# Kernel optimization log

Hardware: AMD Instinct MI355X
Metric: run time of the kernel (lower is better)

Reference implementation:

```python
import jax, jax.numpy as jnp
import numpy as np

EMBED_DIM = 1024
NUM_HEADS = 16
HEAD_DIM = EMBED_DIM // NUM_HEADS


def setup_inputs() -> dict:
    key = jax.random.key(0)
    k_x, k_wqkv, k_bqkv, k_wo, k_bo = jax.random.split(key, 5)
    B, T, C = 8, 1024, EMBED_DIM
    s = 1.0 / np.sqrt(C)
    return {
        "x": jax.random.normal(k_x, (B, T, C), dtype=jnp.float32),
        "W_qkv": jax.random.uniform(k_wqkv, (C, 3 * C), minval=-s, maxval=s, dtype=jnp.float32),
        "b_qkv": jax.random.uniform(k_bqkv, (3 * C,), minval=-s, maxval=s, dtype=jnp.float32),
        "W_out": jax.random.uniform(k_wo, (C, C), minval=-s, maxval=s, dtype=jnp.float32),
        "b_out": jax.random.uniform(k_bo, (C,), minval=-s, maxval=s, dtype=jnp.float32),
    }


def reference(x, W_qkv, b_qkv, W_out, b_out):
    B, T, C = x.shape
    H, D = NUM_HEADS, HEAD_DIM
    qkv = x @ W_qkv + b_qkv                      # [B,T,3C]
    q, k, v = jnp.split(qkv, 3, axis=-1)
    q = q.reshape(B, T, H, D).transpose(0, 2, 1, 3)  # [B,H,T,D]
    k = k.reshape(B, T, H, D).transpose(0, 2, 1, 3)
    v = v.reshape(B, T, H, D).transpose(0, 2, 1, 3)
    scores = jnp.einsum("bhqd,bhkd->bhqk", q, k) / np.sqrt(D).astype(np.float32)
    causal = jnp.tril(jnp.ones((T, T), dtype=bool))
    scores = jnp.where(causal[None, None], scores, -jnp.inf)
    attn = jax.nn.softmax(scores, axis=-1)       # dropout is identity in eval
    out = jnp.einsum("bhqk,bhkd->bhqd", attn, v)
    out = out.transpose(0, 2, 1, 3).reshape(B, T, C)
    return out @ W_out + b_out
```

## Files before the change

kernel.cpp:

```cpp
#include <hip/hip_runtime.h>
#include <hip/hip_bf16.h>
#include <cstdint>

using bf16 = __hip_bfloat16;
typedef short short8 __attribute__((ext_vector_type(8)));
typedef float floatx4 __attribute__((ext_vector_type(4)));

__device__ __forceinline__ void async_load16(const bf16* g, bf16* l) {
    __builtin_amdgcn_global_load_lds(
        (const __attribute__((address_space(1))) uint32_t*)g,
        (__attribute__((address_space(3))) uint32_t*)l, 16, 0, 0);
}

__device__ __forceinline__ uint32_t pack2(float a, float b) {
    union { bf16 h[2]; uint32_t u; } p;
    p.h[0] = __float2bfloat16(a);
    p.h[1] = __float2bfloat16(b);
    return p.u;
}

__global__ __launch_bounds__(256)
void cvt_bf16_kernel(const float* __restrict__ in, bf16* __restrict__ out) {
    const int i = (blockIdx.x * 256 + threadIdx.x) * 4;
    const float4 v = *(const float4*)(in + i);
    bf16 o[4] = {__float2bfloat16(v.x), __float2bfloat16(v.y),
                 __float2bfloat16(v.z), __float2bfloat16(v.w)};
    *(ushort4*)(out + i) = *(ushort4*)o;
}

__global__ __launch_bounds__(256)
void transpose_cvt_kernel(const float* __restrict__ in, bf16* __restrict__ out,
                          int R, int C) {
    __shared__ float tile[32][33];
    const int tx = threadIdx.x & 31, ty = threadIdx.x >> 5;
    const int c0 = blockIdx.x * 32, r0 = blockIdx.y * 32;
    #pragma unroll
    for (int i = 0; i < 32; i += 8)
        tile[ty + i][tx] = in[(size_t)(r0 + ty + i) * C + c0 + tx];
    __syncthreads();
    #pragma unroll
    for (int i = 0; i < 32; i += 8)
        out[(size_t)(c0 + ty + i) * R + r0 + tx] = __float2bfloat16(tile[tx][ty + i]);
}

template <int MODE>
__global__ __launch_bounds__(256, 2)
void gemm_bt_kernel(const bf16* __restrict__ A, const bf16* __restrict__ Bt,
                    const float* __restrict__ bias, int K,
                    bf16* __restrict__ q_ws, bf16* __restrict__ k_ws,
                    bf16* __restrict__ vt_ws, float* __restrict__ out, int N) {
    __shared__ bf16 As[128 * 32];
    __shared__ bf16 Bs[128 * 32];
    const int tid = threadIdx.x;
    const int wave = tid >> 6, lane = tid & 63;
    const int ln = lane & 15, quad = lane >> 4;
    const int wm = wave & 1, wn = wave >> 1;
    const int m0 = blockIdx.y * 128, n0 = blockIdx.x * 128;

    floatx4 acc[4][4] = {};

    for (int k0 = 0; k0 < K; k0 += 32) {
        __syncthreads();
        #pragma unroll
        for (int c = 0; c < 2; ++c) {
            const int e = (c * 256 + tid) * 8;
            async_load16(A + (size_t)(m0 + (e >> 5)) * K + k0 + (e & 31),
                         &As[(c * 256 + wave * 64) * 8]);
        }
        #pragma unroll
        for (int c = 0; c < 2; ++c) {
            const int e = (c * 256 + tid) * 8;
            async_load16(Bt + (size_t)(n0 + (e >> 5)) * K + k0 + (e & 31),
                         &Bs[(c * 256 + wave * 64) * 8]);
        }
        __syncthreads();

        short8 af[4], bfr[4];
        #pragma unroll
        for (int i = 0; i < 4; ++i) {
            af[i]  = *(const short8*)&As[(wm * 64 + i * 16 + ln) * 32 + quad * 8];
            bfr[i] = *(const short8*)&Bs[(wn * 64 + i * 16 + ln) * 32 + quad * 8];
        }
        #pragma unroll
        for (int mi = 0; mi < 4; ++mi)
            #pragma unroll
            for (int ni = 0; ni < 4; ++ni)
                acc[mi][ni] = __builtin_amdgcn_mfma_f32_16x16x32_bf16(
                    af[mi], bfr[ni], acc[mi][ni], 0, 0, 0);
    }

    #pragma unroll
    for (int ni = 0; ni < 4; ++ni) {
        const int col = n0 + wn * 64 + ni * 16 + ln;
        const float bv = bias[col];
        if (MODE == 0) {
            const int which = col >> 10;
            const int cc = col & 1023;
            const int h = cc >> 6, d = cc & 63;
            #pragma unroll
            for (int mi = 0; mi < 4; ++mi) {
                const int rowb = m0 + wm * 64 + mi * 16 + quad * 4;
                if (which == 2) {
                    const int bb = rowb >> 10, t = rowb & 1023;
                    const int tl = t & 63;
                    const int tt = (t & ~63) + ((((tl >> 3) ^ (d & 7)) << 3) | (tl & 7));
                    uint2 w2 = { pack2(acc[mi][ni][0] + bv, acc[mi][ni][1] + bv),
                                 pack2(acc[mi][ni][2] + bv, acc[mi][ni][3] + bv) };
                    *(uint2*)&vt_ws[((size_t)(bb * 16 + h) * 64 + d) * 1024 + tt] = w2;
                } else {
                    bf16* dst = (which == 0) ? q_ws : k_ws;
                    #pragma unroll
                    for (int r = 0; r < 4; ++r) {
                        const int row = rowb + r;
                        const int bb = row >> 10, t = row & 1023;
                        float v = acc[mi][ni][r] + bv;
                        if (which == 0) v *= 0.1803368801111601f;
                        const int dd = (((d >> 3) ^ (t & 7)) << 3) | (d & 7);
                        dst[((size_t)(bb * 16 + h) * 1024 + t) * 64 + dd] =
                            __float2bfloat16(v);
                    }
                }
            }
        } else {
            #pragma unroll
            for (int mi = 0; mi < 4; ++mi) {
                const int rowb = m0 + wm * 64 + mi * 16 + quad * 4;
                #pragma unroll
                for (int r = 0; r < 4; ++r)
                    out[(size_t)(rowb + r) * N + col] = acc[mi][ni][r] + bv;
            }
        }
    }
}

__global__ __launch_bounds__(256, 3)
void attn_kernel(const bf16* __restrict__ Q, const bf16* __restrict__ K,
                 const bf16* __restrict__ Vt, bf16* __restrict__ O) {
    constexpr int T = 1024;
    __shared__ bf16 QPs[128 * 64];
    __shared__ bf16 Ks[2][64 * 64];
    __shared__ bf16 Vts[2][64 * 64];

    const int bh = blockIdx.y;
    const int tid = threadIdx.x;
    const int wave = tid >> 6, lane = tid & 63;
    const int ln = lane & 15, quad = lane >> 4;

    const bf16* Kg = K + (size_t)bh * T * 64;
    const bf16* Vg = Vt + (size_t)bh * 64 * T;
    const int b = bh >> 4, h = bh & 15;

    #pragma unroll
    for (int phase = 0; phase < 2; ++phase) {
        const int jt = phase ? 7 - blockIdx.x : blockIdx.x;
        const int q0 = jt * 128;
        const int nkt = 2 * jt + 2;

        const bf16* Qg = Q + (size_t)bh * T * 64 + (size_t)q0 * 64;
        #pragma unroll
        for (int c = 0; c < 4; ++c)
            async_load16(Qg + (size_t)(c * 256 + tid) * 8,
                         &QPs[(c * 256 + wave * 64) * 8]);
        #pragma unroll
        for (int c = 0; c < 2; ++c)
            async_load16(Kg + (size_t)(c * 256 + tid) * 8,
                         &Ks[0][(c * 256 + wave * 64) * 8]);
        #pragma unroll
        for (int c = 0; c < 2; ++c) {
            const int e = (c * 256 + tid) * 8;
            async_load16(Vg + (size_t)(e >> 6) * T + (e & 63),
                         &Vts[0][(c * 256 + wave * 64) * 8]);
        }
        __syncthreads();

        short8 bq[2][2];
        #pragma unroll
        for (int qj = 0; qj < 2; ++qj)
            #pragma unroll
            for (int ks = 0; ks < 2; ++ks) {
                const int row = wave * 32 + qj * 16 + ln;
                const int ch = (ks * 4 + quad) ^ (row & 7);
                bq[qj][ks] = *(const short8*)&QPs[row * 64 + ch * 8];
            }

        floatx4 oacc[4][2] = {};
        float rm[2] = {-1e30f, -1e30f}, rl[2] = {0.f, 0.f};
        const int qbw = q0 + wave * 32;

        for (int kt = 0; kt < nkt; ++kt) {
            const int cur = kt & 1;
            if (kt + 1 < nkt) {
                const int nxt = cur ^ 1;
                #pragma unroll
                for (int c = 0; c < 2; ++c)
                    async_load16(Kg + (size_t)(kt + 1) * 4096 + (size_t)(c * 256 + tid) * 8,
                                 &Ks[nxt][(c * 256 + wave * 64) * 8]);
                #pragma unroll
                for (int c = 0; c < 2; ++c) {
                    const int e = (c * 256 + tid) * 8;
                    async_load16(Vg + (size_t)(e >> 6) * T + (kt + 1) * 64 + (e & 63),
                                 &Vts[nxt][(c * 256 + wave * 64) * 8]);
                }
            }

            const int k0 = kt * 64;
            if (k0 <= qbw + 31) {
                const bool tail = (k0 + 63 > qbw);

                floatx4 sacc[4][2] = {};
                #pragma unroll
                for (int nj = 0; nj < 4; ++nj) {
                    if (tail && k0 + nj * 16 > qbw + 31) continue;
                    short8 ak[2];
                    #pragma unroll
                    for (int ks = 0; ks < 2; ++ks) {
                        const int row = nj * 16 + ln;
                        const int ch = (ks * 4 + quad) ^ (row & 7);
                        ak[ks] = *(const short8*)&Ks[cur][row * 64 + ch * 8];
                    }
                    #pragma unroll
                    for (int qj = 0; qj < 2; ++qj) {
                        if (tail && k0 + nj * 16 > qbw + qj * 16 + 15) continue;
                        #pragma unroll
                        for (int ks = 0; ks < 2; ++ks)
                            sacc[nj][qj] = __builtin_amdgcn_mfma_f32_16x16x32_bf16(
                                ak[ks], bq[qj][ks], sacc[nj][qj], 0, 0, 0);
                    }
                }

                if (tail) {
                    #pragma unroll
                    for (int nj = 0; nj < 4; ++nj)
                        #pragma unroll
                        for (int qj = 0; qj < 2; ++qj) {
                            const int qq = qbw + qj * 16 + ln;
                            #pragma unroll
                            for (int r = 0; r < 4; ++r) {
                                const int kk = k0 + nj * 16 + quad * 4 + r;
                                if (kk > qq) sacc[nj][qj][r] = -1e30f;
                            }
                        }
                }

                #pragma unroll
                for (int qj = 0; qj < 2; ++qj) {
                    float mx = sacc[0][qj][0];
                    #pragma unroll
                    for (int nj = 0; nj < 4; ++nj)
                        #pragma unroll
                        for (int r = 0; r < 4; ++r) mx = fmaxf(mx, sacc[nj][qj][r]);
                    mx = fmaxf(mx, __shfl_xor(mx, 16, 64));
                    mx = fmaxf(mx, __shfl_xor(mx, 32, 64));
                    const float mn = fmaxf(rm[qj], mx);
                    const float alpha = exp2f(rm[qj] - mn);
                    rm[qj] = mn;
                    rl[qj] *= alpha;
                    #pragma unroll
                    for (int dt = 0; dt < 4; ++dt) oacc[dt][qj] *= alpha;
                    float rs = 0.f;
                    const int qrow = wave * 32 + qj * 16 + ln;
                    #pragma unroll
                    for (int nj = 0; nj < 4; ++nj) {
                        float p[4];
                        #pragma unroll
                        for (int r = 0; r < 4; ++r) {
                            p[r] = exp2f(sacc[nj][qj][r] - mn);
                            rs += p[r];
                        }
                        const int kcol = nj * 16 + quad * 4;
                        const int ch = (kcol >> 3) ^ (qrow & 7);
                        uint2 w2 = { pack2(p[0], p[1]), pack2(p[2], p[3]) };
                        *(uint2*)&QPs[qrow * 64 + ch * 8 + (kcol & 7)] = w2;
                    }
                    rl[qj] += rs;
                }

                #pragma unroll
                for (int ks4 = 0; ks4 < 2; ++ks4) {
                    short8 bp[2];
                    #pragma unroll
                    for (int qj = 0; qj < 2; ++qj) {
                        const int qrow = wave * 32 + qj * 16 + ln;
                        const int ch = (ks4 * 4 + quad) ^ (qrow & 7);
                        bp[qj] = *(const short8*)&QPs[qrow * 64 + ch * 8];
                    }
                    #pragma unroll
                    for (int dt = 0; dt < 4; ++dt) {
                        const int row = dt * 16 + ln;
                        const int ch = (ks4 * 4 + quad) ^ (row & 7);
                        const short8 av = *(const short8*)&Vts[cur][row * 64 + ch * 8];
                        #pragma unroll
                        for (int qj = 0; qj < 2; ++qj)
                            oacc[dt][qj] = __builtin_amdgcn_mfma_f32_16x16x32_bf16(
                                av, bp[qj], oacc[dt][qj], 0, 0, 0);
                    }
                }
            }

            __syncthreads();
        }

        #pragma unroll
        for (int qj = 0; qj < 2; ++qj) {
            float l = rl[qj];
            l += __shfl_xor(l, 16, 64);
            l += __shfl_xor(l, 32, 64);
            const float inv = 1.0f / l;
            const int t = q0 + wave * 32 + qj * 16 + ln;
            const size_t rowb = ((size_t)b * 1024 + t) * 1024 + h * 64;
            #pragma unroll
            for (int dt = 0; dt < 4; ++dt) {
                uint2 w2 = { pack2(oacc[dt][qj][0] * inv, oacc[dt][qj][1] * inv),
                             pack2(oacc[dt][qj][2] * inv, oacc[dt][qj][3] * inv) };
                *(uint2*)&O[rowb + dt * 16 + quad * 4] = w2;
            }
        }
    }
}

extern "C" void kernel_launch(void* const* d_in, const int* in_sizes, int n_in,
                              void* d_out, int out_size, void* d_ws, size_t ws_size,
                              hipStream_t stream) {
    const float* x     = (const float*)d_in[0];
    const float* W_qkv = (const float*)d_in[1];
    const float* b_qkv = (const float*)d_in[2];
    const float* W_out = (const float*)d_in[3];
    const float* b_out = (const float*)d_in[4];
    float* out = (float*)d_out;

    char* ws = (char*)d_ws;
    const size_t MB = 1u << 20;
    bf16* x_bf   = (bf16*)(ws + 0);
    bf16* wqkv_t = (bf16*)(ws + 16 * MB);
    bf16* wout_t = (bf16*)(ws + 22 * MB);
    bf16* q_ws   = (bf16*)(ws + 24 * MB);
    bf16* k_ws   = (bf16*)(ws + 40 * MB);
    bf16* vt_ws  = (bf16*)(ws + 56 * MB);
    bf16* ao_ws  = (bf16*)(ws + 72 * MB);

    cvt_bf16_kernel<<<8192, 256, 0, stream>>>(x, x_bf);
    transpose_cvt_kernel<<<dim3(96, 32), 256, 0, stream>>>(W_qkv, wqkv_t, 1024, 3072);
    transpose_cvt_kernel<<<dim3(32, 32), 256, 0, stream>>>(W_out, wout_t, 1024, 1024);

    gemm_bt_kernel<0><<<dim3(24, 64), 256, 0, stream>>>(
        x_bf, wqkv_t, b_qkv, 1024, q_ws, k_ws, vt_ws, nullptr, 3072);

    attn_kernel<<<dim3(4, 128), 256, 0, stream>>>(q_ws, k_ws, vt_ws, ao_ws);

    gemm_bt_kernel<1><<<dim3(8, 64), 256, 0, stream>>>(
        ao_ws, wout_t, b_out, 1024, nullptr, nullptr, nullptr, out, 1024);
}
```

Before: 252.2 us.

## Double-buffer GEMM tiles, split QKV GEMM, transpose operands for vectorized epilogues

Adds double-buffered LDS staging to the GEMM, using explicit vmcnt/lgkmcnt waits and barriers so the next K tile loads while the current one computes. It also uses the same waits in place of __syncthreads in the attention loop. The QKV projection is split into a Q/K GEMM with swapped operands, computing the transposed product so each lane writes four consecutive head-dim elements as one packed store, plus a separate V GEMM. The output projection is swapped the same way to emit float4 stores. The cost is an extra kernel launch, doubled LDS for the GEMM, and fragile hand-placed wait counts that must match the number of outstanding async loads.

```diff
diff --git a/kernel.cpp b/kernel.cpp
--- a/kernel.cpp
+++ b/kernel.cpp
@@ -5,11 +5,23 @@
 using bf16 = __hip_bfloat16;
 typedef short short8 __attribute__((ext_vector_type(8)));
 typedef float floatx4 __attribute__((ext_vector_type(4)));
+
+#define QSCALE 0.1803368801111601f
 
 __device__ __forceinline__ void async_load16(const bf16* g, bf16* l) {
     __builtin_amdgcn_global_load_lds(
         (const __attribute__((address_space(1))) uint32_t*)g,
         (__attribute__((address_space(3))) uint32_t*)l, 16, 0, 0);
+}
+
+__device__ __forceinline__ void bar_lgkm0() {
+    asm volatile("s_waitcnt lgkmcnt(0)\ns_barrier" ::: "memory");
+}
+__device__ __forceinline__ void bar_vm4() {
+    asm volatile("s_waitcnt vmcnt(4)\ns_barrier" ::: "memory");
+}
+__device__ __forceinline__ void bar_vm0() {
+    asm volatile("s_waitcnt vmcnt(0)\ns_barrier" ::: "memory");
 }
 
 __device__ __forceinline__ uint32_t pack2(float a, float b) {
@@ -44,13 +56,13 @@
 }
 
 template <int MODE>
-__global__ __launch_bounds__(256, 2)
+__global__ __launch_bounds__(256, 4)
 void gemm_bt_kernel(const bf16* __restrict__ A, const bf16* __restrict__ Bt,
                     const float* __restrict__ bias, int K,
-                    bf16* __restrict__ q_ws, bf16* __restrict__ k_ws,
-                    bf16* __restrict__ vt_ws, float* __restrict__ out, int N) {
-    __shared__ bf16 As[128 * 32];
-    __shared__ bf16 Bs[128 * 32];
+                    bf16* __restrict__ o0, bf16* __restrict__ o1,
+                    float* __restrict__ fout) {
+    __shared__ bf16 As[2][128 * 32];
+    __shared__ bf16 Bs[2][128 * 32];
     const int tid = threadIdx.x;
     const int wave = tid >> 6, lane = tid & 63;
     const int ln = lane & 15, quad = lane >> 4;
@@ -58,28 +70,48 @@
     const int m0 = blockIdx.y * 128, n0 = blockIdx.x * 128;
 
     floatx4 acc[4][4] = {};
-
-    for (int k0 = 0; k0 < K; k0 += 32) {
-        __syncthreads();
-        #pragma unroll
-        for (int c = 0; c < 2; ++c) {
-            const int e = (c * 256 + tid) * 8;
-            async_load16(A + (size_t)(m0 + (e >> 5)) * K + k0 + (e & 31),
-                         &As[(c * 256 + wave * 64) * 8]);
-        }
-        #pragma unroll
-        for (int c = 0; c < 2; ++c) {
-            const int e = (c * 256 + tid) * 8;
-            async_load16(Bt + (size_t)(n0 + (e >> 5)) * K + k0 + (e & 31),
-                         &Bs[(c * 256 + wave * 64) * 8]);
-        }
-        __syncthreads();
+    const int nkt = K >> 5;
+
+    #pragma unroll
+    for (int c = 0; c < 2; ++c) {
+        const int e = (c * 256 + tid) * 8;
+        async_load16(A + (size_t)(m0 + (e >> 5)) * K + (e & 31),
+                     &As[0][(c * 256 + wave * 64) * 8]);
+    }
+    #pragma unroll
+    for (int c = 0; c < 2; ++c) {
+        const int e = (c * 256 + tid) * 8;
+        async_load16(Bt + (size_t)(n0 + (e >> 5)) * K + (e & 31),
+                     &Bs[0][(c * 256 + wave * 64) * 8]);
+    }
+
+    for (int kt = 0; kt < nkt; ++kt) {
+        const int cur = kt & 1;
+        bar_lgkm0();
+        if (kt + 1 < nkt) {
+            const int k0 = (kt + 1) << 5;
+            #pragma unroll
+            for (int c = 0; c < 2; ++c) {
+                const int e = (c * 256 + tid) * 8;
+                async_load16(A + (size_t)(m0 + (e >> 5)) * K + k0 + (e & 31),
+                             &As[cur ^ 1][(c * 256 + wave * 64) * 8]);
+            }
+            #pragma unroll
+            for (int c = 0; c < 2; ++c) {
+                const int e = (c * 256 + tid) * 8;
+                async_load16(Bt + (size_t)(n0 + (e >> 5)) * K + k0 + (e & 31),
+                             &Bs[cur ^ 1][(c * 256 + wave * 64) * 8]);
+            }
+            bar_vm4();
+        } else {
+            bar_vm0();
+        }
 
         short8 af[4], bfr[4];
         #pragma unroll
         for (int i = 0; i < 4; ++i) {
-            af[i]  = *(const short8*)&As[(wm * 64 + i * 16 + ln) * 32 + quad * 8];
-            bfr[i] = *(const short8*)&Bs[(wn * 64 + i * 16 + ln) * 32 + quad * 8];
+            af[i]  = *(const short8*)&As[cur][(wm * 64 + i * 16 + ln) * 32 + quad * 8];
+            bfr[i] = *(const short8*)&Bs[cur][(wn * 64 + i * 16 + ln) * 32 + quad * 8];
         }
         #pragma unroll
         for (int mi = 0; mi < 4; ++mi)
@@ -89,45 +121,56 @@
                     af[mi], bfr[ni], acc[mi][ni], 0, 0, 0);
     }
 
-    #pragma unroll
-    for (int ni = 0; ni < 4; ++ni) {
-        const int col = n0 + wn * 64 + ni * 16 + ln;
-        const float bv = bias[col];
-        if (MODE == 0) {
-            const int which = col >> 10;
-            const int cc = col & 1023;
-            const int h = cc >> 6, d = cc & 63;
+    if (MODE == 0) {
+        #pragma unroll
+        for (int mi = 0; mi < 4; ++mi) {
+            const int ch0 = m0 + wm * 64 + mi * 16 + quad * 4;
+            const int which = ch0 >> 10;
+            const int h = (ch0 & 1023) >> 6, d0 = ch0 & 63;
+            const float4 bv = *(const float4*)&bias[ch0];
+            bf16* dst = which ? o1 : o0;
+            #pragma unroll
+            for (int ni = 0; ni < 4; ++ni) {
+                const int tok = n0 + wn * 64 + ni * 16 + ln;
+                const int bb = tok >> 10, t = tok & 1023;
+                float v0 = acc[mi][ni][0] + bv.x;
+                float v1 = acc[mi][ni][1] + bv.y;
+                float v2 = acc[mi][ni][2] + bv.z;
+                float v3 = acc[mi][ni][3] + bv.w;
+                if (which == 0) { v0 *= QSCALE; v1 *= QSCALE; v2 *= QSCALE; v3 *= QSCALE; }
+                const int dd = (((d0 >> 3) ^ (t & 7)) << 3) | (d0 & 7);
+                uint2 w2 = { pack2(v0, v1), pack2(v2, v3) };
+                *(uint2*)&dst[((size_t)(bb * 16 + h) * 1024 + t) * 64 + dd] = w2;
+            }
+        }
+    } else if (MODE == 2) {
+        #pragma unroll
+        for (int ni = 0; ni < 4; ++ni) {
+            const int col = n0 + wn * 64 + ni * 16 + ln;
+            const int h = col >> 6, d = col & 63;
+            const float bv = bias[col];
             #pragma unroll
             for (int mi = 0; mi < 4; ++mi) {
                 const int rowb = m0 + wm * 64 + mi * 16 + quad * 4;
-                if (which == 2) {
-                    const int bb = rowb >> 10, t = rowb & 1023;
-                    const int tl = t & 63;
-                    const int tt = (t & ~63) + ((((tl >> 3) ^ (d & 7)) << 3) | (tl & 7));
-                    uint2 w2 = { pack2(acc[mi][ni][0] + bv, acc[mi][ni][1] + bv),
-                                 pack2(acc[mi][ni][2] + bv, acc[mi][ni][3] + bv) };
-                    *(uint2*)&vt_ws[((size_t)(bb * 16 + h) * 64 + d) * 1024 + tt] = w2;
-                } else {
-                    bf16* dst = (which == 0) ? q_ws : k_ws;
-                    #pragma unroll
-                    for (int r = 0; r < 4; ++r) {
-                        const int row = rowb + r;
-                        const int bb = row >> 10, t = row & 1023;
-                        float v = acc[mi][ni][r] + bv;
-                        if (which == 0) v *= 0.1803368801111601f;
-                        const int dd = (((d >> 3) ^ (t & 7)) << 3) | (d & 7);
-                        dst[((size_t)(bb * 16 + h) * 1024 + t) * 64 + dd] =
-                            __float2bfloat16(v);
-                    }
-                }
-            }
-        } else {
-            #pragma unroll
-            for (int mi = 0; mi < 4; ++mi) {
-                const int rowb = m0 + wm * 64 + mi * 16 + quad * 4;
-                #pragma unroll
-                for (int r = 0; r < 4; ++r)
-                    out[(size_t)(rowb + r) * N + col] = acc[mi][ni][r] + bv;
+                const int bb = rowb >> 10, t = rowb & 1023;
+                const int tl = t & 63;
+                const int tt = (t & ~63) + ((((tl >> 3) ^ (d & 7)) << 3) | (tl & 7));
+                uint2 w2 = { pack2(acc[mi][ni][0] + bv, acc[mi][ni][1] + bv),
+                             pack2(acc[mi][ni][2] + bv, acc[mi][ni][3] + bv) };
+                *(uint2*)&o0[((size_t)(bb * 16 + h) * 64 + d) * 1024 + tt] = w2;
+            }
+        }
+    } else {
+        #pragma unroll
+        for (int mi = 0; mi < 4; ++mi) {
+            const int ch0 = m0 + wm * 64 + mi * 16 + quad * 4;
+            const float4 bv = *(const float4*)&bias[ch0];
+            #pragma unroll
+            for (int ni = 0; ni < 4; ++ni) {
+                const int tok = n0 + wn * 64 + ni * 16 + ln;
+                float4 o = { acc[mi][ni][0] + bv.x, acc[mi][ni][1] + bv.y,
+                             acc[mi][ni][2] + bv.z, acc[mi][ni][3] + bv.w };
+                *(float4*)&fout[(size_t)tok * 1024 + ch0] = o;
             }
         }
     }
@@ -156,6 +199,8 @@
         const int q0 = jt * 128;
         const int nkt = 2 * jt + 2;
 
+        bar_lgkm0();
+
         const bf16* Qg = Q + (size_t)bh * T * 64 + (size_t)q0 * 64;
         #pragma unroll
         for (int c = 0; c < 4; ++c)
@@ -171,7 +216,7 @@
             async_load16(Vg + (size_t)(e >> 6) * T + (e & 63),
                          &Vts[0][(c * 256 + wave * 64) * 8]);
         }
-        __syncthreads();
+        bar_vm0();
 
         short8 bq[2][2];
         #pragma unroll
@@ -189,6 +234,7 @@
 
         for (int kt = 0; kt < nkt; ++kt) {
             const int cur = kt & 1;
+            bar_lgkm0();
             if (kt + 1 < nkt) {
                 const int nxt = cur ^ 1;
                 #pragma unroll
@@ -201,103 +247,103 @@
                     async_load16(Vg + (size_t)(e >> 6) * T + (kt + 1) * 64 + (e & 63),
                                  &Vts[nxt][(c * 256 + wave * 64) * 8]);
                 }
+                bar_vm4();
+            } else {
+                bar_vm0();
             }
 
             const int k0 = kt * 64;
-            if (k0 <= qbw + 31) {
-                const bool tail = (k0 + 63 > qbw);
-
-                floatx4 sacc[4][2] = {};
-                #pragma unroll
-                for (int nj = 0; nj < 4; ++nj) {
-                    if (tail && k0 + nj * 16 > qbw + 31) continue;
-                    short8 ak[2];
+            if (k0 > qbw + 31) continue;
+            const bool tail = (k0 + 63 > qbw);
+
+            floatx4 sacc[4][2] = {};
+            #pragma unroll
+            for (int nj = 0; nj < 4; ++nj) {
+                if (tail && k0 + nj * 16 > qbw + 31) continue;
+                short8 ak[2];
+                #pragma unroll
+                for (int ks = 0; ks < 2; ++ks) {
+                    const int row = nj * 16 + ln;
+                    const int ch = (ks * 4 + quad) ^ (row & 7);
+                    ak[ks] = *(const short8*)&Ks[cur][row * 64 + ch * 8];
+                }
+                #pragma unroll
+                for (int qj = 0; qj < 2; ++qj) {
+                    if (tail && k0 + nj * 16 > qbw + qj * 16 + 15) continue;
                     #pragma unroll
-                    for (int ks = 0; ks < 2; ++ks) {
-                        const int row = nj * 16 + ln;
-                        const int ch = (ks * 4 + quad) ^ (row & 7);
-                        ak[ks] = *(const short8*)&Ks[cur][row * 64 + ch * 8];
-                    }
+                    for (int ks = 0; ks < 2; ++ks)
+                        sacc[nj][qj] = __builtin_amdgcn_mfma_f32_16x16x32_bf16(
+                            ak[ks], bq[qj][ks], sacc[nj][qj], 0, 0, 0);
+                }
+            }
+
+            if (tail) {
+                #pragma unroll
+                for (int nj = 0; nj < 4; ++nj)
                     #pragma unroll
                     for (int qj = 0; qj < 2; ++qj) {
-                        if (tail && k0 + nj * 16 > qbw + qj * 16 + 15) continue;
-                        #pragma unroll
-                        for (int ks = 0; ks < 2; ++ks)
-                            sacc[nj][qj] = __builtin_amdgcn_mfma_f32_16x16x32_bf16(
-                                ak[ks], bq[qj][ks], sacc[nj][qj], 0, 0, 0);
-                    }
-                }
-
-                if (tail) {
-                    #pragma unroll
-                    for (int nj = 0; nj < 4; ++nj)
-                        #pragma unroll
-                        for (int qj = 0; qj < 2; ++qj) {
-                            const int qq = qbw + qj * 16 + ln;
-                            #pragma unroll
-                            for (int r = 0; r < 4; ++r) {
-                                const int kk = k0 + nj * 16 + quad * 4 + r;
-                                if (kk > qq) sacc[nj][qj][r] = -1e30f;
-                            }
-                        }
-                }
-
-                #pragma unroll
-                for (int qj = 0; qj < 2; ++qj) {
-                    float mx = sacc[0][qj][0];
-                    #pragma unroll
-                    for (int nj = 0; nj < 4; ++nj)
-                        #pragma unroll
-                        for (int r = 0; r < 4; ++r) mx = fmaxf(mx, sacc[nj][qj][r]);
-                    mx = fmaxf(mx, __shfl_xor(mx, 16, 64));
-                    mx = fmaxf(mx, __shfl_xor(mx, 32, 64));
-                    const float mn = fmaxf(rm[qj], mx);
-                    const float alpha = exp2f(rm[qj] - mn);
-                    rm[qj] = mn;
-                    rl[qj] *= alpha;
-                    #pragma unroll
-                    for (int dt = 0; dt < 4; ++dt) oacc[dt][qj] *= alpha;
-                    float rs = 0.f;
-                    const int qrow = wave * 32 + qj * 16 + ln;
-                    #pragma unroll
-                    for (int nj = 0; nj < 4; ++nj) {
-                        float p[4];
+                        const int qq = qbw + qj * 16 + ln;
                         #pragma unroll
                         for (int r = 0; r < 4; ++r) {
-                            p[r] = exp2f(sacc[nj][qj][r] - mn);
-                            rs += p[r];
+                            const int kk = k0 + nj * 16 + quad * 4 + r;
+                            if (kk > qq) sacc[nj][qj][r] = -1e30f;
                         }
-                        const int kcol = nj * 16 + quad * 4;
-                        const int ch = (kcol >> 3) ^ (qrow & 7);
-                        uint2 w2 = { pack2(p[0], p[1]), pack2(p[2], p[3]) };
-                        *(uint2*)&QPs[qrow * 64 + ch * 8 + (kcol & 7)] = w2;
                     }
-                    rl[qj] += rs;
-                }
-
-                #pragma unroll
-                for (int ks4 = 0; ks4 < 2; ++ks4) {
-                    short8 bp[2];
+            }
+
+            #pragma unroll
+            for (int qj = 0; qj < 2; ++qj) {
+                float mx = sacc[0][qj][0];
+                #pragma unroll
+                for (int nj = 0; nj < 4; ++nj)
                     #pragma unroll
-                    for (int qj = 0; qj < 2; ++qj) {
-                        const int qrow = wave * 32 + qj * 16 + ln;
-                        const int ch = (ks4 * 4 + quad) ^ (qrow & 7);
-                        bp[qj] = *(const short8*)&QPs[qrow * 64 + ch * 8];
+                    for (int r = 0; r < 4; ++r) mx = fmaxf(mx, sacc[nj][qj][r]);
+                mx = fmaxf(mx, __shfl_xor(mx, 16, 64));
+                mx = fmaxf(mx, __shfl_xor(mx, 32, 64));
+                const float mn = fmaxf(rm[qj], mx);
+                const float alpha = exp2f(rm[qj] - mn);
+                rm[qj] = mn;
+                rl[qj] *= alpha;
+                #pragma unroll
+                for (int dt = 0; dt < 4; ++dt) oacc[dt][qj] *= alpha;
+                float rs = 0.f;
+                const int qrow = wave * 32 + qj * 16 + ln;
+                #pragma unroll
+                for (int nj = 0; nj < 4; ++nj) {
+                    float p[4];
+                    #pragma unroll
+                    for (int r = 0; r < 4; ++r) {
+                        p[r] = exp2f(sacc[nj][qj][r] - mn);
+                        rs += p[r];
                     }
+                    const int kcol = nj * 16 + quad * 4;
+                    const int ch = (kcol >> 3) ^ (qrow & 7);
+                    uint2 w2 = { pack2(p[0], p[1]), pack2(p[2], p[3]) };
+                    *(uint2*)&QPs[qrow * 64 + ch * 8 + (kcol & 7)] = w2;
+                }
+                rl[qj] += rs;
+            }
+
+            #pragma unroll
+            for (int ks4 = 0; ks4 < 2; ++ks4) {
+                short8 bp[2];
+                #pragma unroll
+                for (int qj = 0; qj < 2; ++qj) {
+                    const int qrow = wave * 32 + qj * 16 + ln;
+                    const int ch = (ks4 * 4 + quad) ^ (qrow & 7);
+                    bp[qj] = *(const short8*)&QPs[qrow * 64 + ch * 8];
+                }
+                #pragma unroll
+                for (int dt = 0; dt < 4; ++dt) {
+                    const int row = dt * 16 + ln;
+                    const int ch = (ks4 * 4 + quad) ^ (row & 7);
+                    const short8 av = *(const short8*)&Vts[cur][row * 64 + ch * 8];
                     #pragma unroll
-                    for (int dt = 0; dt < 4; ++dt) {
-                        const int row = dt * 16 + ln;
-                        const int ch = (ks4 * 4 + quad) ^ (row & 7);
-                        const short8 av = *(const short8*)&Vts[cur][row * 64 + ch * 8];
-                        #pragma unroll
-                        for (int qj = 0; qj < 2; ++qj)
-                            oacc[dt][qj] = __builtin_amdgcn_mfma_f32_16x16x32_bf16(
-                                av, bp[qj], oacc[dt][qj], 0, 0, 0);
-                    }
-                }
-            }
-
-            __syncthreads();
+                    for (int qj = 0; qj < 2; ++qj)
+                        oacc[dt][qj] = __builtin_amdgcn_mfma_f32_16x16x32_bf16(
+                            av, bp[qj], oacc[dt][qj], 0, 0, 0);
+                }
+            }
         }
 
         #pragma unroll
@@ -342,11 +388,13 @@
     transpose_cvt_kernel<<<dim3(96, 32), 256, 0, stream>>>(W_qkv, wqkv_t, 1024, 3072);
     transpose_cvt_kernel<<<dim3(32, 32), 256, 0, stream>>>(W_out, wout_t, 1024, 1024);
 
-    gemm_bt_kernel<0><<<dim3(24, 64), 256, 0, stream>>>(
-        x_bf, wqkv_t, b_qkv, 1024, q_ws, k_ws, vt_ws, nullptr, 3072);
+    gemm_bt_kernel<0><<<dim3(64, 16), 256, 0, stream>>>(
+        wqkv_t, x_bf, b_qkv, 1024, q_ws, k_ws, nullptr);
+    gemm_bt_kernel<2><<<dim3(8, 64), 256, 0, stream>>>(
+        x_bf, wqkv_t + (size_t)2048 * 1024, b_qkv + 2048, 1024, vt_ws, nullptr, nullptr);
 
     attn_kernel<<<dim3(4, 128), 256, 0, stream>>>(q_ws, k_ws, vt_ws, ao_ws);
 
-    gemm_bt_kernel<1><<<dim3(8, 64), 256, 0, stream>>>(
-        ao_ws, wout_t, b_out, 1024, nullptr, nullptr, nullptr, out, 1024);
-}
+    gemm_bt_kernel<1><<<dim3(64, 8), 256, 0, stream>>>(
+        wout_t, ao_ws, b_out, 1024, nullptr, nullptr, out);
+}
```

New measurement: 255.2 us. No clear change (+1.2%).
